# Performance work log

Hardware: AMD Instinct MI355X
Metric: run time of the kernel (lower is better)

## Reference

```python
import math
import jax, jax.numpy as jnp
import numpy as np

BATCH = 16384
N = 2048            # in_size = out_size, power of 2
LOG_N = 11          # log2(N)
NSTACKS = 1
NBLOCKS = 1


def setup_inputs() -> dict:
    key = jax.random.key(0)
    k1, k2, k3 = jax.random.split(key, 3)
    x = jax.random.normal(k1, (BATCH, N), jnp.float32)
    # init='randn': twiddle ~ N(0,1) / sqrt(2)
    twiddle = jax.random.normal(
        k2, (NSTACKS, NBLOCKS, LOG_N, N // 2, 2, 2), jnp.float32) / jnp.sqrt(jnp.float32(2.0))
    bound = 1.0 / math.sqrt(N)  # nn.Linear-style bias init, in_size = N
    bias = jax.random.uniform(k3, (N,), jnp.float32, -bound, bound)
    return {"x": x, "twiddle": twiddle, "bias": bias}


def butterfly_multiply(twiddle, x, increasing_stride=True):
    # twiddle: (S, n_blocks, log_n, n//2, 2, 2);  x: (B, S, n)
    B, S, n = x.shape
    n_blocks, log_n = twiddle.shape[1], twiddle.shape[2]
    out = x
    cur = increasing_stride
    for block in range(n_blocks):
        for idx in range(log_n):
            log_stride = idx if cur else log_n - 1 - idx
            s = 1 << log_stride
            g = n // (2 * s)  # number of butterfly groups at this stride
            # t: (S, g, s, 2, 2); pair axis j contracts against input halves
            t = twiddle[:, block, idx].reshape(S, g, s, 2, 2)
            xr = out.reshape(B, S, g, 2, s)
            out = jnp.einsum('kgsij,bkgjs->bkgis', t, xr).reshape(B, S, n)
        cur = not cur
    return out


def reference(x, twiddle, bias):
    B = x.shape[0]
    # pre_process: flatten batch dims, expand over nstacks
    out = jnp.broadcast_to(x[:, None, :], (B, NSTACKS, N))
    out = butterfly_multiply(twiddle, out, increasing_stride=True)
    # post_process: flatten stacks, truncate to out_size, add bias
    out = out.reshape(B, NSTACKS * N)[:, :N] + bias
    return out
```

## Files before the change

### kernel.cpp

```cpp
#include <hip/hip_runtime.h>


constexpr int BATCH = 16384;
constexpr int N = 2048;
constexpr int ROWS = 4;
constexpr int WPB = 4;
constexpr int BLOCK = 64 * WPB;
constexpr int GRID = BATCH / (ROWS * WPB);

#define SCHED_FENCE() asm volatile("" ::: "memory")

template <int M>
__device__ __forceinline__ float part_xor(float x) {
    if constexpr (M == 1)
        return __int_as_float(__builtin_amdgcn_mov_dpp(__float_as_int(x), 0xB1, 0xF, 0xF, true));
    else if constexpr (M == 2)
        return __int_as_float(__builtin_amdgcn_mov_dpp(__float_as_int(x), 0x4E, 0xF, 0xF, true));
    else if constexpr (M == 4)
        return __int_as_float(__builtin_amdgcn_ds_swizzle(__float_as_int(x), 0x101F));
    else if constexpr (M == 8)
        return __int_as_float(__builtin_amdgcn_ds_swizzle(__float_as_int(x), 0x201F));
    else if constexpr (M == 16)
        return __int_as_float(__builtin_amdgcn_ds_swizzle(__float_as_int(x), 0x401F));
    else
        return __shfl_xor(x, 32, 64);
}

template <int ST>
__device__ __forceinline__ void mid_stage(float (&v)[ROWS][32], const float* twst, int lane) {
    constexpr int s = 1 << ST;
    constexpr int m = 1 << (ST - 1);
    const int hiHalf = (lane >> (ST - 1)) & 1;
    const int l2 = lane * 2;
    #pragma unroll
    for (int k = 0; k < 32; ++k) {
        const int e = (k >> 1) * 128 + l2 + (k & 1);
        const int p = ((e >> (ST + 1)) << ST) | (e & (s - 1));
        const float2 t2 = *(const float2*)(twst + 4 * p + 2 * hiHalf);
        const float cm = hiHalf ? t2.y : t2.x;
        const float cp = hiHalf ? t2.x : t2.y;
        #pragma unroll
        for (int rr = 0; rr < ROWS; ++rr) {
            const float mine = v[rr][k];
            const float part = part_xor<m>(mine);
            v[rr][k] = fmaf(cm, mine, cp * part);
        }
        if ((k & 7) == 7) SCHED_FENCE();
    }
}

template <int ST>
__device__ __forceinline__ void hi_stage(float (&v)[ROWS][32], const float* twst, int lane) {
    constexpr int s = 1 << ST;
    constexpr int rm = 1 << (ST - 7);
    const int l2 = lane * 2;
    #pragma unroll
    for (int r = 0; r < 16; ++r) {
        if (r & rm) continue;
        #pragma unroll
        for (int j = 0; j < 2; ++j) {
            const int e = r * 128 + l2 + j;
            const int p = ((e >> (ST + 1)) << ST) | (e & (s - 1));
            const float4 t4 = *(const float4*)(twst + 4 * p);
            const int klo = 2 * r + j;
            const int khi = 2 * (r + rm) + j;
            #pragma unroll
            for (int rr = 0; rr < ROWS; ++rr) {
                const float lo = v[rr][klo];
                const float hi = v[rr][khi];
                v[rr][klo] = fmaf(t4.x, lo, t4.y * hi);
                v[rr][khi] = fmaf(t4.z, lo, t4.w * hi);
            }
        }
        if ((r & 1) == 1) SCHED_FENCE();
    }
}

__global__ __launch_bounds__(BLOCK, 1)
void butterfly_kernel(const float* __restrict__ x,
                      const float* __restrict__ tw,
                      const float* __restrict__ bias,
                      float* __restrict__ out)
{
    const int tid = threadIdx.x;
    const int lane = tid & 63;
    const int w = tid >> 6;
    const int wid = blockIdx.x * WPB + w;
    const size_t row0 = (size_t)wid * ROWS;
    const int l2 = lane * 2;

    float v[ROWS][32];

    #pragma unroll
    for (int rr = 0; rr < ROWS; ++rr) {
        const float* src = x + (row0 + rr) * N + l2;
        #pragma unroll
        for (int r = 0; r < 16; ++r) {
            const float2 f = *(const float2*)(src + r * 128);
            v[rr][2*r]   = f.x;
            v[rr][2*r+1] = f.y;
        }
    }

    #pragma unroll
    for (int r = 0; r < 16; ++r) {
        const float4 t4 = *(const float4*)(tw + 4 * (r * 64 + lane));
        #pragma unroll
        for (int rr = 0; rr < ROWS; ++rr) {
            const float lo = v[rr][2*r];
            const float hi = v[rr][2*r+1];
            v[rr][2*r]   = fmaf(t4.x, lo, t4.y * hi);
            v[rr][2*r+1] = fmaf(t4.z, lo, t4.w * hi);
        }
        if ((r & 3) == 3) SCHED_FENCE();
    }

    mid_stage<1>(v, tw + (1 << 12), lane);
    mid_stage<2>(v, tw + (2 << 12), lane);
    mid_stage<3>(v, tw + (3 << 12), lane);
    mid_stage<4>(v, tw + (4 << 12), lane);
    mid_stage<5>(v, tw + (5 << 12), lane);
    mid_stage<6>(v, tw + (6 << 12), lane);

    hi_stage<7>(v, tw + (7 << 12), lane);
    hi_stage<8>(v, tw + (8 << 12), lane);
    hi_stage<9>(v, tw + (9 << 12), lane);
    hi_stage<10>(v, tw + (10 << 12), lane);

    #pragma unroll
    for (int r = 0; r < 16; ++r) {
        const float2 b = *(const float2*)(bias + r * 128 + l2);
        #pragma unroll
        for (int rr = 0; rr < ROWS; ++rr) {
            float2 o;
            o.x = v[rr][2*r]   + b.x;
            o.y = v[rr][2*r+1] + b.y;
            *(float2*)(out + (row0 + rr) * N + r * 128 + l2) = o;
        }
    }
}

extern "C" void kernel_launch(void* const* d_in, const int* in_sizes, int n_in,
                              void* d_out, int out_size, void* d_ws, size_t ws_size,
                              hipStream_t stream) {
    const float* x    = (const float*)d_in[0];
    const float* tw   = (const float*)d_in[1];
    const float* bias = (const float*)d_in[2];
    float* out = (float*)d_out;

    butterfly_kernel<<<GRID, BLOCK, 0, stream>>>(x, tw, bias, out);
}
```

Before: 323.4 us.

## Process one row per wave with float4 lane layout and two in-register stages

Each wave now handles one row instead of four, and each lane owns four consecutive elements per 256-wide chunk. This makes stages 0 and 1 purely in-register, moves stage 7 to the cross-lane path, and uses float4 loads and stores. The launch bound goes to 2 blocks per CU to raise occupancy. In exchange, each twiddle load is now amortized over one row instead of four, so twiddle traffic per output rises roughly fourfold.

```diff
diff --git a/kernel.cpp b/kernel.cpp
--- a/kernel.cpp
+++ b/kernel.cpp
@@ -3,10 +3,9 @@
 
 constexpr int BATCH = 16384;
 constexpr int N = 2048;
-constexpr int ROWS = 4;
 constexpr int WPB = 4;
 constexpr int BLOCK = 64 * WPB;
-constexpr int GRID = BATCH / (ROWS * WPB);
+constexpr int GRID = BATCH / WPB;
 
 #define SCHED_FENCE() asm volatile("" ::: "memory")
 
@@ -27,56 +26,49 @@
 }
 
 template <int ST>
-__device__ __forceinline__ void mid_stage(float (&v)[ROWS][32], const float* twst, int lane) {
+__device__ __forceinline__ void mid_stage(float (&v)[32], const float* twst, int lane) {
     constexpr int s = 1 << ST;
-    constexpr int m = 1 << (ST - 1);
-    const int hiHalf = (lane >> (ST - 1)) & 1;
-    const int l2 = lane * 2;
+    constexpr int m = 1 << (ST - 2);
+    const int h = (lane >> (ST - 2)) & 1;
+    const int l4 = lane * 4;
     #pragma unroll
     for (int k = 0; k < 32; ++k) {
-        const int e = (k >> 1) * 128 + l2 + (k & 1);
+        const int e = (k >> 2) * 256 + l4 + (k & 3);
         const int p = ((e >> (ST + 1)) << ST) | (e & (s - 1));
-        const float2 t2 = *(const float2*)(twst + 4 * p + 2 * hiHalf);
-        const float cm = hiHalf ? t2.y : t2.x;
-        const float cp = hiHalf ? t2.x : t2.y;
-        #pragma unroll
-        for (int rr = 0; rr < ROWS; ++rr) {
-            const float mine = v[rr][k];
-            const float part = part_xor<m>(mine);
-            v[rr][k] = fmaf(cm, mine, cp * part);
-        }
-        if ((k & 7) == 7) SCHED_FENCE();
+        const float2 t2 = *(const float2*)(twst + 4 * p + 2 * h);
+        const float cm = h ? t2.y : t2.x;
+        const float cp = h ? t2.x : t2.y;
+        const float part = part_xor<m>(v[k]);
+        v[k] = fmaf(cm, v[k], cp * part);
+        if ((k & 3) == 3) SCHED_FENCE();
     }
 }
 
 template <int ST>
-__device__ __forceinline__ void hi_stage(float (&v)[ROWS][32], const float* twst, int lane) {
+__device__ __forceinline__ void hi_stage(float (&v)[32], const float* twst, int lane) {
     constexpr int s = 1 << ST;
-    constexpr int rm = 1 << (ST - 7);
-    const int l2 = lane * 2;
+    constexpr int rm = 1 << (ST - 8);
+    const int l4 = lane * 4;
     #pragma unroll
-    for (int r = 0; r < 16; ++r) {
+    for (int r = 0; r < 8; ++r) {
         if (r & rm) continue;
         #pragma unroll
-        for (int j = 0; j < 2; ++j) {
-            const int e = r * 128 + l2 + j;
+        for (int jj = 0; jj < 4; ++jj) {
+            const int e = r * 256 + l4 + jj;
             const int p = ((e >> (ST + 1)) << ST) | (e & (s - 1));
             const float4 t4 = *(const float4*)(twst + 4 * p);
-            const int klo = 2 * r + j;
-            const int khi = 2 * (r + rm) + j;
-            #pragma unroll
-            for (int rr = 0; rr < ROWS; ++rr) {
-                const float lo = v[rr][klo];
-                const float hi = v[rr][khi];
-                v[rr][klo] = fmaf(t4.x, lo, t4.y * hi);
-                v[rr][khi] = fmaf(t4.z, lo, t4.w * hi);
-            }
+            const int klo = 4 * r + jj;
+            const int khi = 4 * (r + rm) + jj;
+            const float lo = v[klo];
+            const float hi = v[khi];
+            v[klo] = fmaf(t4.x, lo, t4.y * hi);
+            v[khi] = fmaf(t4.z, lo, t4.w * hi);
+            if ((jj & 1) == 1) SCHED_FENCE();
         }
-        if ((r & 1) == 1) SCHED_FENCE();
     }
 }
 
-__global__ __launch_bounds__(BLOCK, 1)
+__global__ __launch_bounds__(BLOCK, 2)
 void butterfly_kernel(const float* __restrict__ x,
                       const float* __restrict__ tw,
                       const float* __restrict__ bias,
@@ -85,58 +77,75 @@
     const int tid = threadIdx.x;
     const int lane = tid & 63;
     const int w = tid >> 6;
-    const int wid = blockIdx.x * WPB + w;
-    const size_t row0 = (size_t)wid * ROWS;
-    const int l2 = lane * 2;
+    const size_t row = (size_t)blockIdx.x * WPB + w;
+    const int l4 = lane * 4;
 
-    float v[ROWS][32];
+    float v[32];
+
+    const float* src = x + row * N + l4;
+    #pragma unroll
+    for (int r = 0; r < 8; ++r) {
+        const float4 f = *(const float4*)(src + r * 256);
+        v[4*r]   = f.x;
+        v[4*r+1] = f.y;
+        v[4*r+2] = f.z;
+        v[4*r+3] = f.w;
+    }
 
     #pragma unroll
-    for (int rr = 0; rr < ROWS; ++rr) {
-        const float* src = x + (row0 + rr) * N + l2;
+    for (int r = 0; r < 8; ++r) {
         #pragma unroll
-        for (int r = 0; r < 16; ++r) {
-            const float2 f = *(const float2*)(src + r * 128);
-            v[rr][2*r]   = f.x;
-            v[rr][2*r+1] = f.y;
+        for (int jh = 0; jh < 2; ++jh) {
+            const int p = r * 128 + lane * 2 + jh;
+            const float4 t4 = *(const float4*)(tw + 4 * p);
+            const int klo = 4 * r + 2 * jh;
+            const float lo = v[klo];
+            const float hi = v[klo + 1];
+            v[klo]     = fmaf(t4.x, lo, t4.y * hi);
+            v[klo + 1] = fmaf(t4.z, lo, t4.w * hi);
+        }
+        if (r & 1) SCHED_FENCE();
+    }
+
+    {
+        const float* tw1 = tw + 4096;
+        #pragma unroll
+        for (int r = 0; r < 8; ++r) {
+            #pragma unroll
+            for (int jl = 0; jl < 2; ++jl) {
+                const int p = r * 128 + lane * 2 + jl;
+                const float4 t4 = *(const float4*)(tw1 + 4 * p);
+                const int klo = 4 * r + jl;
+                const float lo = v[klo];
+                const float hi = v[klo + 2];
+                v[klo]     = fmaf(t4.x, lo, t4.y * hi);
+                v[klo + 2] = fmaf(t4.z, lo, t4.w * hi);
+            }
+            if (r & 1) SCHED_FENCE();
         }
     }
 
-    #pragma unroll
-    for (int r = 0; r < 16; ++r) {
-        const float4 t4 = *(const float4*)(tw + 4 * (r * 64 + lane));
-        #pragma unroll
-        for (int rr = 0; rr < ROWS; ++rr) {
-            const float lo = v[rr][2*r];
-            const float hi = v[rr][2*r+1];
-            v[rr][2*r]   = fmaf(t4.x, lo, t4.y * hi);
-            v[rr][2*r+1] = fmaf(t4.z, lo, t4.w * hi);
-        }
-        if ((r & 3) == 3) SCHED_FENCE();
-    }
-
-    mid_stage<1>(v, tw + (1 << 12), lane);
     mid_stage<2>(v, tw + (2 << 12), lane);
     mid_stage<3>(v, tw + (3 << 12), lane);
     mid_stage<4>(v, tw + (4 << 12), lane);
     mid_stage<5>(v, tw + (5 << 12), lane);
     mid_stage<6>(v, tw + (6 << 12), lane);
+    mid_stage<7>(v, tw + (7 << 12), lane);
 
-    hi_stage<7>(v, tw + (7 << 12), lane);
-    hi_stage<8>(v, tw + (8 << 12), lane);
-    hi_stage<9>(v, tw + (9 << 12), lane);
+    hi_stage<8>(v,  tw + (8 << 12), lane);
+    hi_stage<9>(v,  tw + (9 << 12), lane);
     hi_stage<10>(v, tw + (10 << 12), lane);
 
+    float* dst = out + row * N + l4;
     #pragma unroll
-    for (int r = 0; r < 16; ++r) {
-        const float2 b = *(const float2*)(bias + r * 128 + l2);
-        #pragma unroll
-        for (int rr = 0; rr < ROWS; ++rr) {
-            float2 o;
-            o.x = v[rr][2*r]   + b.x;
-            o.y = v[rr][2*r+1] + b.y;
-            *(float2*)(out + (row0 + rr) * N + r * 128 + l2) = o;
-        }
+    for (int r = 0; r < 8; ++r) {
+        const float4 b = *(const float4*)(bias + r * 256 + l4);
+        float4 o;
+        o.x = v[4*r]   + b.x;
+        o.y = v[4*r+1] + b.y;
+        o.z = v[4*r+2] + b.z;
+        o.w = v[4*r+3] + b.w;
+        *(float4*)(dst + r * 256) = o;
     }
 }
 
```

New measurement: 391.9 us. 21.2% more time.
